# Optimization experiments

Measured on AMD Instinct MI355X. Metric: run time of the kernel, lower is better.

## Reference

```python
import jax, jax.numpy as jnp
import numpy as np

B, T, D, H = 64, 1024, 256, 256
DROP_P = 0.5


def setup_inputs() -> dict:
    key = jax.random.key(0)
    ks = jax.random.split(key, 14)
    s = 1.0 / np.sqrt(H)
    inp = {
        "x": jax.random.normal(ks[0], (B, T, D), jnp.float32),
        "W_f": jax.random.normal(ks[1], (D, 4 * H), jnp.float32) * s,
        "U_f": jax.random.normal(ks[2], (H, 4 * H), jnp.float32) * s,
        "b_f": jnp.zeros((4 * H,), jnp.float32),
        "pi_f": jax.random.normal(ks[3], (H,), jnp.float32) * s,
        "pf_f": jax.random.normal(ks[4], (H,), jnp.float32) * s,
        "po_f": jax.random.normal(ks[5], (H,), jnp.float32) * s,
        "W_b": jax.random.normal(ks[6], (D, 4 * H), jnp.float32) * s,
        "U_b": jax.random.normal(ks[7], (H, 4 * H), jnp.float32) * s,
        "b_b": jnp.zeros((4 * H,), jnp.float32),
        "pi_b": jax.random.normal(ks[8], (H,), jnp.float32) * s,
        "pf_b": jax.random.normal(ks[9], (H,), jnp.float32) * s,
        "po_b": jax.random.normal(ks[10], (H,), jnp.float32) * s,
    }
    return inp


def _peephole_lstm_dir(x, W, U, b, pi, pf, po, reverse):
    # Precompute input projection for all timesteps: [B,T,4H]
    xW = jnp.einsum('btd,dg->btg', x, W) + b
    if reverse:
        xW = xW[:, ::-1]
    h0 = jnp.zeros((x.shape[0], H), x.dtype)
    c0 = jnp.zeros((x.shape[0], H), x.dtype)

    def step(carry, xw_t):
        h, c = carry
        g = xw_t + h @ U                       # [B,4H]
        gi, gf, gg, go = jnp.split(g, 4, axis=-1)
        i = jax.nn.sigmoid(gi + pi * c)        # peephole on c_{t-1}
        f = jax.nn.sigmoid(gf + pf * c)
        c_new = f * c + i * jnp.tanh(gg)
        o = jax.nn.sigmoid(go + po * c_new)    # peephole on c_t
        h_new = o * jnp.tanh(c_new)
        return (h_new, c_new), h_new

    _, hs = jax.lax.scan(step, (h0, c0), jnp.swapaxes(xW, 0, 1))  # [T,B,H]
    hs = jnp.swapaxes(hs, 0, 1)  # [B,T,H]
    if reverse:
        hs = hs[:, ::-1]
    return hs


def reference(x, W_f, U_f, b_f, pi_f, pf_f, po_f, W_b, U_b, b_b, pi_b, pf_b, po_b):
    h_fwd = _peephole_lstm_dir(x, W_f, U_f, b_f, pi_f, pf_f, po_f, reverse=False)
    h_bwd = _peephole_lstm_dir(x, W_b, U_b, b_b, pi_b, pf_b, po_b, reverse=True)
    out = jnp.concatenate([h_fwd, h_bwd], axis=-1)  # [B,T,2H]
    # training-mode dropout with a fixed key (deterministic for baselining)
    keep = jax.random.bernoulli(jax.random.key(42), 1.0 - DROP_P, out.shape)
    out = jnp.where(keep, out / (1.0 - DROP_P), 0.0)
    return out
```

## Files before the change

### kernel.cpp

```cpp
#include <hip/hip_runtime.h>

typedef unsigned int uint;
typedef unsigned short ushort;
typedef unsigned long long u64;
typedef short bf16x8 __attribute__((ext_vector_type(8)));
typedef float f32x4 __attribute__((ext_vector_type(4)));

#define XW_OFF   0ull
#define XB_OFF   (XW_OFF + 268435456ull)
#define WT_OFF   (XB_OFF + 33554432ull)
#define UT_OFF   (WT_OFF + 1048576ull)
#define WS_NEED  (UT_OFF + 1048576ull)

static __device__ __forceinline__ ushort f2bf(float f) {
  uint u = __float_as_uint(f);
  return (ushort)((u + 0x7fffu + ((u >> 16) & 1u)) >> 16);
}
static __device__ __forceinline__ float bf2f(ushort s) {
  return __uint_as_float((uint)s << 16);
}
static __device__ __forceinline__ float fsig(float x) {
  return 1.0f / (1.0f + __expf(-x));
}
static __device__ __forceinline__ float ftanh(float x) {
  return 1.0f - 2.0f / (__expf(2.0f * x) + 1.0f);
}

static __device__ __forceinline__ void gload_lds16(const void* g, void* l) {
  auto gp = (const __attribute__((address_space(1))) uint*)((const void*)g);
  auto lp = (__attribute__((address_space(3))) uint*)((void*)l);
  __builtin_amdgcn_global_load_lds(gp, lp, 16, 0, 0);
}

__global__ __launch_bounds__(256) void k_convert(
    const float* __restrict__ x,
    const float* __restrict__ Wf, const float* __restrict__ Wb,
    const float* __restrict__ Uf, const float* __restrict__ Ub,
    ushort* __restrict__ xb, ushort* __restrict__ wt, ushort* __restrict__ ut)
{
  uint tid = blockIdx.x * 256u + threadIdx.x;
  if (tid < 2097152u) {
    uint base = tid * 8u;
    float4 a = *(const float4*)(x + base);
    float4 b = *(const float4*)(x + base + 4);
    uint4 o;
    o.x = (uint)f2bf(a.x) | ((uint)f2bf(a.y) << 16);
    o.y = (uint)f2bf(a.z) | ((uint)f2bf(a.w) << 16);
    o.z = (uint)f2bf(b.x) | ((uint)f2bf(b.y) << 16);
    o.w = (uint)f2bf(b.z) | ((uint)f2bf(b.w) << 16);
    *(uint4*)(xb + base) = o;
  } else {
    uint e = tid - 2097152u;
    uint which = e >> 18;
    uint i = e & 262143u;
    uint n = i >> 8, k = i & 255u;
    uint orig = (n & 3u) * 256u + (n >> 2);
    const float* src = (which == 0) ? Wf : (which == 1) ? Wb : (which == 2) ? Uf : Ub;
    ushort v = f2bf(src[k * 1024u + orig]);
    ushort* dst = (which < 2) ? (wt + which * 262144u) : (ut + (which - 2u) * 262144u);
    dst[n * 256u + k] = v;
  }
}

__global__ __launch_bounds__(256) void k_gemm(
    const ushort* __restrict__ xb, const ushort* __restrict__ wt,
    const float* __restrict__ biasF, const float* __restrict__ biasB,
    ushort* __restrict__ xw2)
{
  const int dir = blockIdx.z;
  const ushort* W = wt + dir * 262144;
  const float* bias = dir ? biasB : biasF;
  const int m0 = blockIdx.x * 128;
  const int n0 = blockIdx.y * 128;
  const int tid = threadIdx.x;
  const int lane = tid & 63, wave = tid >> 6;
  const int l15 = lane & 15, l4 = lane >> 4;
  const int wr = wave >> 1, wc = wave & 1;

  __shared__ __align__(16) ushort lds[17664];
  ushort* As = lds;
  ushort* Bs = lds + 5120;

  f32x4 acc[4][4] = {};
  const int arow = tid >> 1, aseg = tid & 1;

  for (int kit = 0; kit < 8; ++kit) {
    int k0 = kit * 32;
    const ushort* sa = xb + (m0 + arow) * 256 + k0 + aseg * 16;
    uint4 a0 = *(const uint4*)sa;
    uint4 a1 = *(const uint4*)(sa + 8);
    const ushort* sb = W + (n0 + arow) * 256 + k0 + aseg * 16;
    uint4 b0 = *(const uint4*)sb;
    uint4 b1 = *(const uint4*)(sb + 8);
    *(uint4*)(As + arow * 40 + aseg * 16) = a0;
    *(uint4*)(As + arow * 40 + aseg * 16 + 8) = a1;
    *(uint4*)(Bs + arow * 40 + aseg * 16) = b0;
    *(uint4*)(Bs + arow * 40 + aseg * 16 + 8) = b1;
    __syncthreads();
    bf16x8 af[4], bfr[4];
#pragma unroll
    for (int m = 0; m < 4; ++m) af[m] = *(const bf16x8*)(As + (wr * 64 + m * 16 + l15) * 40 + l4 * 8);
#pragma unroll
    for (int n = 0; n < 4; ++n) bfr[n] = *(const bf16x8*)(Bs + (wc * 64 + n * 16 + l15) * 40 + l4 * 8);
#pragma unroll
    for (int m = 0; m < 4; ++m)
#pragma unroll
      for (int n = 0; n < 4; ++n)
        acc[m][n] = __builtin_amdgcn_mfma_f32_16x16x32_bf16(af[m], bfr[n], acc[m][n], 0, 0, 0);
    __syncthreads();
  }

  float bv[4];
#pragma unroll
  for (int n = 0; n < 4; ++n) {
    int colp = n0 + wc * 64 + n * 16 + l15;
    bv[n] = bias[(colp & 3) * 256 + (colp >> 2)];
  }
  ushort* tl = lds;
#pragma unroll
  for (int m = 0; m < 4; ++m)
#pragma unroll
    for (int n = 0; n < 4; ++n) {
      int col = wc * 64 + n * 16 + l15;
#pragma unroll
      for (int r = 0; r < 4; ++r) {
        int trow = wr * 64 + m * 16 + l4 * 4 + r;
        tl[trow * 136 + col] = f2bf(acc[m][n][r] + bv[n]);
      }
    }
  __syncthreads();

  const int b = m0 >> 10;
  const int bgrp = b >> 2, b_loc = b & 3;
  const int t0 = m0 & 1023;
#pragma unroll
  for (int it = 0; it < 8; ++it) {
    int idx = it * 256 + tid;
    int row = idx >> 4, ch = idx & 15;
    uint4 v = *(const uint4*)(tl + row * 136 + ch * 8);
    u64 off = ((u64)((dir * 16 + bgrp) * 1024 + (t0 + row))) * 4096ull
              + (u64)(b_loc * 1024 + n0 + ch * 8);
    *(uint4*)(xw2 + off) = v;
  }
}

__global__ __launch_bounds__(1024) void k_rec(
    const ushort* __restrict__ xw2, const ushort* __restrict__ ut,
    const float* __restrict__ pif, const float* __restrict__ pff, const float* __restrict__ pof,
    const float* __restrict__ pib, const float* __restrict__ pfb, const float* __restrict__ pob,
    float* __restrict__ out)
{
  const int bid = blockIdx.x;
  const int dir = bid >> 4;
  const int bgrp = bid & 15;
  const int tid = threadIdx.x;
  const int lane = tid & 63, wv = tid >> 6;
  const int l15 = lane & 15, l4 = lane >> 4;
  const int u = wv * 16 + l15;

  __shared__ __align__(16) ushort uld[65536];
  __shared__ __align__(16) ushort hst[2176];
  __shared__ __align__(16) ushort xsl[12288];

  const float* piP = dir ? pib : pif;
  const float* pfP = dir ? pfb : pff;
  const float* poP = dir ? pob : pof;
  const float ppi = piP[u], ppf = pfP[u], ppo = poP[u];

  const ushort* U = ut + dir * 262144;
  bf16x8 ufr[6][4];
#pragma unroll
  for (int g = 0; g < 4; ++g) {
    const ushort* up = U + (u * 4 + g) * 256;
#pragma unroll
    for (int kt = 0; kt < 6; ++kt)
      ufr[kt][g] = *(const bf16x8*)(up + kt * 32 + l4 * 8);
#pragma unroll
    for (int kt = 6; kt < 8; ++kt)
      *(bf16x8*)(uld + wv * 4096 + ((kt - 6) * 4 + g) * 512 + lane * 8) =
          *(const bf16x8*)(up + kt * 32 + l4 * 8);
  }
  for (int i = tid; i < 2176; i += 1024) hst[i] = 0;

  const ushort* xwbase = xw2 + (u64)(dir * 16 + bgrp) * 1024ull * 4096ull;

  if (tid < 512) {
    const ushort* s0 = xwbase + (u64)(dir ? 1023 : 0) * 4096ull + (uint)tid * 8u;
    const ushort* s1 = xwbase + (u64)(dir ? 1022 : 1) * 4096ull + (uint)tid * 8u;
    gload_lds16(s0, &xsl[(tid >> 6) * 512]);
    gload_lds16(s1, &xsl[4096 + (tid >> 6) * 512]);
  }
  asm volatile("s_waitcnt vmcnt(0) lgkmcnt(0)" ::: "memory");
  __syncthreads();

  float cr = 0.f;
  float* outp = out + ((u64)(bgrp * 4 + l4) * 1024ull) * 512ull + (u64)(dir * 256 + u);
  int scur = 0;

  for (int t = 0; t < 1024; ++t) {
    if (t + 2 < 1024 && tid < 512) {
      const int snxt = (scur >= 1) ? (scur - 1) : 2;
      const ushort* src = xwbase + (u64)(dir ? 1021 - t : t + 2) * 4096ull + (uint)tid * 8u;
      gload_lds16(src, &xsl[snxt * 4096 + (tid >> 6) * 512]);
    }

    const ushort* sA = hst + ((t + 1) & 1) * 1088 + (l15 >> 2) * 272 + l4 * 8;
    f32x4 acc0 = {0.f, 0.f, 0.f, 0.f}, acc1 = acc0, acc2 = acc0, acc3 = acc0;
#pragma unroll
    for (int kt = 0; kt < 6; ++kt) {
      bf16x8 a = *(const bf16x8*)(sA + kt * 32);
      acc0 = __builtin_amdgcn_mfma_f32_16x16x32_bf16(a, ufr[kt][0], acc0, 0, 0, 0);
      acc1 = __builtin_amdgcn_mfma_f32_16x16x32_bf16(a, ufr[kt][1], acc1, 0, 0, 0);
      acc2 = __builtin_amdgcn_mfma_f32_16x16x32_bf16(a, ufr[kt][2], acc2, 0, 0, 0);
      acc3 = __builtin_amdgcn_mfma_f32_16x16x32_bf16(a, ufr[kt][3], acc3, 0, 0, 0);
    }
#pragma unroll
    for (int kt = 6; kt < 8; ++kt) {
      bf16x8 a = *(const bf16x8*)(sA + kt * 32);
      const ushort* ub = uld + wv * 4096 + (kt - 6) * 2048 + lane * 8;
      acc0 = __builtin_amdgcn_mfma_f32_16x16x32_bf16(a, *(const bf16x8*)(ub), acc0, 0, 0, 0);
      acc1 = __builtin_amdgcn_mfma_f32_16x16x32_bf16(a, *(const bf16x8*)(ub + 512), acc1, 0, 0, 0);
      acc2 = __builtin_amdgcn_mfma_f32_16x16x32_bf16(a, *(const bf16x8*)(ub + 1024), acc2, 0, 0, 0);
      acc3 = __builtin_amdgcn_mfma_f32_16x16x32_bf16(a, *(const bf16x8*)(ub + 1536), acc3, 0, 0, 0);
    }

    u64 xv = *(const u64*)(xsl + scur * 4096 + (l4 << 10) + (u << 2));
    {
      float cc = cr;
      float gi = acc0[0] + bf2f((ushort)xv);
      float gf = acc1[0] + bf2f((ushort)(xv >> 16));
      float gg = acc2[0] + bf2f((ushort)(xv >> 32));
      float go = acc3[0] + bf2f((ushort)(xv >> 48));
      float iv = fsig(gi + ppi * cc);
      float fv = fsig(gf + ppf * cc);
      float cn = fv * cc + iv * ftanh(gg);
      float ov = fsig(go + ppo * cn);
      float h = ov * ftanh(cn);
      cr = cn;
      hst[(t & 1) * 1088 + l4 * 272 + u] = f2bf(h);
      const int tout = dir ? (1023 - t) : t;
      __builtin_nontemporal_store(h, outp + (u64)tout * 512ull);
    }

    asm volatile("s_waitcnt vmcnt(2) lgkmcnt(0)\n\ts_barrier" ::: "memory");
    scur = (scur == 2) ? 0 : (scur + 1);
  }
}

#define TFR(r) { x0 += x1; x1 = (x1 << (r)) | (x1 >> (32 - (r))); x1 ^= x0; }
#define RND4A TFR(13) TFR(15) TFR(26) TFR(6)
#define RND4B TFR(17) TFR(29) TFR(16) TFR(24)

static __device__ __forceinline__ void threefry(uint c0, uint c1, uint& y0, uint& y1) {
  const uint k0 = 0u, k1 = 42u;
  const uint ks2 = k0 ^ k1 ^ 0x1BD11BDAu;
  uint x0 = c0 + k0, x1 = c1 + k1;
  RND4A x0 += k1;  x1 += ks2 + 1u;
  RND4B x0 += ks2; x1 += k0 + 2u;
  RND4A x0 += k0;  x1 += k1 + 3u;
  RND4B x0 += k1;  x1 += ks2 + 4u;
  RND4A x0 += ks2; x1 += k0 + 5u;
  y0 = x0; y1 = x1;
}

__global__ __launch_bounds__(256) void k_drop(float* out, uint n) {
  uint i = blockIdx.x * 256u + threadIdx.x;
  if (i < n) {
    uint y0, y1;
    threefry(0u, i, y0, y1);
    uint w = y0 ^ y1;
    float v = out[i];
    out[i] = (w >> 31) ? 0.0f : v * 2.0f;
  }
}

extern "C" void kernel_launch(void* const* d_in, const int* in_sizes, int n_in,
                              void* d_out, int out_size, void* d_ws, size_t ws_size,
                              hipStream_t stream)
{
  const float* x   = (const float*)d_in[0];
  const float* Wf  = (const float*)d_in[1];
  const float* Uf  = (const float*)d_in[2];
  const float* bf_ = (const float*)d_in[3];
  const float* pif = (const float*)d_in[4];
  const float* pff = (const float*)d_in[5];
  const float* pof = (const float*)d_in[6];
  const float* Wb  = (const float*)d_in[7];
  const float* Ub  = (const float*)d_in[8];
  const float* bb_ = (const float*)d_in[9];
  const float* pib = (const float*)d_in[10];
  const float* pfb = (const float*)d_in[11];
  const float* pob = (const float*)d_in[12];
  float* out = (float*)d_out;
  char* ws = (char*)d_ws;

  if (ws_size < WS_NEED) {
    hipMemsetAsync(d_out, 0, (size_t)out_size * 4, stream);
    return;
  }

  ushort* xwp = (ushort*)(ws + XW_OFF);
  ushort* xbp = (ushort*)(ws + XB_OFF);
  ushort* wtp = (ushort*)(ws + WT_OFF);
  ushort* utp = (ushort*)(ws + UT_OFF);

  k_convert<<<12288, 256, 0, stream>>>(x, Wf, Wb, Uf, Ub, xbp, wtp, utp);
  k_gemm<<<dim3(512, 8, 2), 256, 0, stream>>>(xbp, wtp, bf_, bb_, xwp);
  k_rec<<<32, 1024, 0, stream>>>(xwp, utp, pif, pff, pof, pib, pfb, pob, out);
  k_drop<<<(out_size + 255) / 256, 256, 0, stream>>>(out, (uint)out_size);
}
```

Before: 2.647 ms.

## Keep all recurrent weights in registers and prefetch xW directly into registers

The full U slice (all 8 k-tiles across 4 gates) is now held in VGPRs instead of splitting 2 k-tiles into LDS. The async global-to-LDS triple buffer for the precomputed input projection is replaced by a two-deep per-thread register prefetch. The timestep loop is unrolled by two, and output stores become ordinary stores instead of nontemporal ones. The aim is to drop LDS reads of U and xW from the serial critical path. With 1024-thread blocks, the extra 32 VGPRs of weights per thread risks spilling to scratch, which would sit inside the recurrence loop.

```diff
diff --git a/kernel.cpp b/kernel.cpp
--- a/kernel.cpp
+++ b/kernel.cpp
@@ -24,12 +24,6 @@
 }
 static __device__ __forceinline__ float ftanh(float x) {
   return 1.0f - 2.0f / (__expf(2.0f * x) + 1.0f);
-}
-
-static __device__ __forceinline__ void gload_lds16(const void* g, void* l) {
-  auto gp = (const __attribute__((address_space(1))) uint*)((const void*)g);
-  auto lp = (__attribute__((address_space(3))) uint*)((void*)l);
-  __builtin_amdgcn_global_load_lds(gp, lp, 16, 0, 0);
 }
 
 __global__ __launch_bounds__(256) void k_convert(
@@ -154,13 +148,11 @@
   const int dir = bid >> 4;
   const int bgrp = bid & 15;
   const int tid = threadIdx.x;
-  const int lane = tid & 63, wv = tid >> 6;
+  const int lane = tid & 63;
   const int l15 = lane & 15, l4 = lane >> 4;
-  const int u = wv * 16 + l15;
-
-  __shared__ __align__(16) ushort uld[65536];
+  const int u = (tid >> 6) * 16 + l15;
+
   __shared__ __align__(16) ushort hst[2176];
-  __shared__ __align__(16) ushort xsl[12288];
 
   const float* piP = dir ? pib : pif;
   const float* pfP = dir ? pfb : pff;
@@ -168,82 +160,67 @@
   const float ppi = piP[u], ppf = pfP[u], ppo = poP[u];
 
   const ushort* U = ut + dir * 262144;
-  bf16x8 ufr[6][4];
+  bf16x8 ufr[8][4];
 #pragma unroll
   for (int g = 0; g < 4; ++g) {
     const ushort* up = U + (u * 4 + g) * 256;
 #pragma unroll
-    for (int kt = 0; kt < 6; ++kt)
+    for (int kt = 0; kt < 8; ++kt)
       ufr[kt][g] = *(const bf16x8*)(up + kt * 32 + l4 * 8);
-#pragma unroll
-    for (int kt = 6; kt < 8; ++kt)
-      *(bf16x8*)(uld + wv * 4096 + ((kt - 6) * 4 + g) * 512 + lane * 8) =
-          *(const bf16x8*)(up + kt * 32 + l4 * 8);
   }
   for (int i = tid; i < 2176; i += 1024) hst[i] = 0;
-
-  const ushort* xwbase = xw2 + (u64)(dir * 16 + bgrp) * 1024ull * 4096ull;
-
-  if (tid < 512) {
-    const ushort* s0 = xwbase + (u64)(dir ? 1023 : 0) * 4096ull + (uint)tid * 8u;
-    const ushort* s1 = xwbase + (u64)(dir ? 1022 : 1) * 4096ull + (uint)tid * 8u;
-    gload_lds16(s0, &xsl[(tid >> 6) * 512]);
-    gload_lds16(s1, &xsl[4096 + (tid >> 6) * 512]);
-  }
-  asm volatile("s_waitcnt vmcnt(0) lgkmcnt(0)" ::: "memory");
   __syncthreads();
 
+  const ushort* xp = xw2 + (u64)(dir * 16 + bgrp) * 4194304ull
+                     + (uint)(l4 * 1024 + u * 4);
   float cr = 0.f;
   float* outp = out + ((u64)(bgrp * 4 + l4) * 1024ull) * 512ull + (u64)(dir * 256 + u);
-  int scur = 0;
-
-  for (int t = 0; t < 1024; ++t) {
-    if (t + 2 < 1024 && tid < 512) {
-      const int snxt = (scur >= 1) ? (scur - 1) : 2;
-      const ushort* src = xwbase + (u64)(dir ? 1021 - t : t + 2) * 4096ull + (uint)tid * 8u;
-      gload_lds16(src, &xsl[snxt * 4096 + (tid >> 6) * 512]);
-    }
-
+
+  u64 pa = *(const u64*)(xp + (u64)(dir ? 1023 : 0) * 4096ull);
+  u64 pb = *(const u64*)(xp + (u64)(dir ? 1022 : 1) * 4096ull);
+
+  auto step = [&](u64 xv, int t) {
     const ushort* sA = hst + ((t + 1) & 1) * 1088 + (l15 >> 2) * 272 + l4 * 8;
     f32x4 acc0 = {0.f, 0.f, 0.f, 0.f}, acc1 = acc0, acc2 = acc0, acc3 = acc0;
 #pragma unroll
-    for (int kt = 0; kt < 6; ++kt) {
+    for (int kt = 0; kt < 8; ++kt) {
       bf16x8 a = *(const bf16x8*)(sA + kt * 32);
       acc0 = __builtin_amdgcn_mfma_f32_16x16x32_bf16(a, ufr[kt][0], acc0, 0, 0, 0);
       acc1 = __builtin_amdgcn_mfma_f32_16x16x32_bf16(a, ufr[kt][1], acc1, 0, 0, 0);
       acc2 = __builtin_amdgcn_mfma_f32_16x16x32_bf16(a, ufr[kt][2], acc2, 0, 0, 0);
       acc3 = __builtin_amdgcn_mfma_f32_16x16x32_bf16(a, ufr[kt][3], acc3, 0, 0, 0);
     }
-#pragma unroll
-    for (int kt = 6; kt < 8; ++kt) {
-      bf16x8 a = *(const bf16x8*)(sA + kt * 32);
-      const ushort* ub = uld + wv * 4096 + (kt - 6) * 2048 + lane * 8;
-      acc0 = __builtin_amdgcn_mfma_f32_16x16x32_bf16(a, *(const bf16x8*)(ub), acc0, 0, 0, 0);
-      acc1 = __builtin_amdgcn_mfma_f32_16x16x32_bf16(a, *(const bf16x8*)(ub + 512), acc1, 0, 0, 0);
-      acc2 = __builtin_amdgcn_mfma_f32_16x16x32_bf16(a, *(const bf16x8*)(ub + 1024), acc2, 0, 0, 0);
-      acc3 = __builtin_amdgcn_mfma_f32_16x16x32_bf16(a, *(const bf16x8*)(ub + 1536), acc3, 0, 0, 0);
-    }
-
-    u64 xv = *(const u64*)(xsl + scur * 4096 + (l4 << 10) + (u << 2));
+    float cc = cr;
+    float gi = acc0[0] + bf2f((ushort)xv);
+    float gf = acc1[0] + bf2f((ushort)(xv >> 16));
+    float gg = acc2[0] + bf2f((ushort)(xv >> 32));
+    float go = acc3[0] + bf2f((ushort)(xv >> 48));
+    float iv = fsig(gi + ppi * cc);
+    float fv = fsig(gf + ppf * cc);
+    float cn = fv * cc + iv * ftanh(gg);
+    float ov = fsig(go + ppo * cn);
+    float h = ov * ftanh(cn);
+    cr = cn;
+    hst[(t & 1) * 1088 + l4 * 272 + u] = f2bf(h);
+    const int tout = dir ? (1023 - t) : t;
+    outp[(u64)tout * 512ull] = h;
+  };
+
+  for (int t = 0; t < 1024; t += 2) {
     {
-      float cc = cr;
-      float gi = acc0[0] + bf2f((ushort)xv);
-      float gf = acc1[0] + bf2f((ushort)(xv >> 16));
-      float gg = acc2[0] + bf2f((ushort)(xv >> 32));
-      float go = acc3[0] + bf2f((ushort)(xv >> 48));
-      float iv = fsig(gi + ppi * cc);
-      float fv = fsig(gf + ppf * cc);
-      float cn = fv * cc + iv * ftanh(gg);
-      float ov = fsig(go + ppo * cn);
-      float h = ov * ftanh(cn);
-      cr = cn;
-      hst[(t & 1) * 1088 + l4 * 272 + u] = f2bf(h);
-      const int tout = dir ? (1023 - t) : t;
-      __builtin_nontemporal_store(h, outp + (u64)tout * 512ull);
-    }
-
-    asm volatile("s_waitcnt vmcnt(2) lgkmcnt(0)\n\ts_barrier" ::: "memory");
-    scur = (scur == 2) ? 0 : (scur + 1);
+      u64 xv = pa;
+      if (t + 2 < 1024)
+        pa = *(const u64*)(xp + (u64)(dir ? 1021 - t : t + 2) * 4096ull);
+      step(xv, t);
+      asm volatile("s_waitcnt vmcnt(2) lgkmcnt(0)\n\ts_barrier" ::: "memory");
+    }
+    {
+      u64 xv = pb;
+      if (t + 3 < 1024)
+        pb = *(const u64*)(xp + (u64)(dir ? 1020 - t : t + 3) * 4096ull);
+      step(xv, t + 1);
+      asm volatile("s_waitcnt vmcnt(2) lgkmcnt(0)\n\ts_barrier" ::: "memory");
+    }
   }
 }
 
```

New measurement: 5.825 ms. 120% more time.

## Halve recurrent block to 512 threads, keep full U slice in registers

Applied to the files above, without the earlier changes.

The recurrent kernel now runs 8 waves per block instead of 16, and each wave handles 32 hidden units with 8 MFMA accumulators. The entire U slice (8x8 bf16x8 fragments per lane) lives in registers, which removes the LDS-resident part of U and its per-step LDS reads. The U transpose layout in the convert kernel is changed to match the new wave-to-unit mapping, and the xW prefetch is moved after the gate math with a waitcnt adjusted to match. The cost is much higher register pressure (launch_bounds 512,2) and half as many waves to hide latency in the serial loop, with the output store changed from nontemporal to a plain store.

```diff
diff --git a/kernel.cpp b/kernel.cpp
--- a/kernel.cpp
+++ b/kernel.cpp
@@ -54,7 +54,13 @@
     uint which = e >> 18;
     uint i = e & 262143u;
     uint n = i >> 8, k = i & 255u;
-    uint orig = (n & 3u) * 256u + (n >> 2);
+    uint orig;
+    if (which < 2) {
+      orig = (n & 3u) * 256u + (n >> 2);
+    } else {
+      uint w = n >> 7, nn = (n >> 4) & 7u, c = n & 15u;
+      orig = (nn & 3u) * 256u + w * 32u + ((nn >> 2) << 4) + c;
+    }
     const float* src = (which == 0) ? Wf : (which == 1) ? Wb : (which == 2) ? Uf : Ub;
     ushort v = f2bf(src[k * 1024u + orig]);
     ushort* dst = (which < 2) ? (wt + which * 262144u) : (ut + (which - 2u) * 262144u);
@@ -144,7 +150,7 @@
   }
 }
 
-__global__ __launch_bounds__(1024) void k_rec(
+__global__ __launch_bounds__(512, 2) void k_rec(
     const ushort* __restrict__ xw2, const ushort* __restrict__ ut,
     const float* __restrict__ pif, const float* __restrict__ pff, const float* __restrict__ pof,
     const float* __restrict__ pib, const float* __restrict__ pfb, const float* __restrict__ pob,
@@ -156,35 +162,32 @@
   const int tid = threadIdx.x;
   const int lane = tid & 63, wv = tid >> 6;
   const int l15 = lane & 15, l4 = lane >> 4;
-  const int u = wv * 16 + l15;
-
-  __shared__ __align__(16) ushort uld[65536];
+  const int u0 = wv * 32 + l15;
+  const int u1 = u0 + 16;
+
   __shared__ __align__(16) ushort hst[2176];
   __shared__ __align__(16) ushort xsl[12288];
 
   const float* piP = dir ? pib : pif;
   const float* pfP = dir ? pfb : pff;
   const float* poP = dir ? pob : pof;
-  const float ppi = piP[u], ppf = pfP[u], ppo = poP[u];
+  const float pi0 = piP[u0], pf0 = pfP[u0], po0 = poP[u0];
+  const float pi1 = piP[u1], pf1 = pfP[u1], po1 = poP[u1];
 
   const ushort* U = ut + dir * 262144;
-  bf16x8 ufr[6][4];
-#pragma unroll
-  for (int g = 0; g < 4; ++g) {
-    const ushort* up = U + (u * 4 + g) * 256;
-#pragma unroll
-    for (int kt = 0; kt < 6; ++kt)
-      ufr[kt][g] = *(const bf16x8*)(up + kt * 32 + l4 * 8);
-#pragma unroll
-    for (int kt = 6; kt < 8; ++kt)
-      *(bf16x8*)(uld + wv * 4096 + ((kt - 6) * 4 + g) * 512 + lane * 8) =
-          *(const bf16x8*)(up + kt * 32 + l4 * 8);
-  }
-  for (int i = tid; i < 2176; i += 1024) hst[i] = 0;
-
-  const ushort* xwbase = xw2 + (u64)(dir * 16 + bgrp) * 1024ull * 4096ull;
-
-  if (tid < 512) {
+  bf16x8 ufr[8][8];
+#pragma unroll
+  for (int n = 0; n < 8; ++n) {
+    const ushort* up = U + (wv * 128 + n * 16 + l15) * 256;
+#pragma unroll
+    for (int kt = 0; kt < 8; ++kt)
+      ufr[kt][n] = *(const bf16x8*)(up + kt * 32 + l4 * 8);
+  }
+  for (int i = tid; i < 2176; i += 512) hst[i] = 0;
+
+  const ushort* xwbase = xw2 + (u64)(dir * 16 + bgrp) * 4194304ull;
+
+  {
     const ushort* s0 = xwbase + (u64)(dir ? 1023 : 0) * 4096ull + (uint)tid * 8u;
     const ushort* s1 = xwbase + (u64)(dir ? 1022 : 1) * 4096ull + (uint)tid * 8u;
     gload_lds16(s0, &xsl[(tid >> 6) * 512]);
@@ -193,57 +196,70 @@
   asm volatile("s_waitcnt vmcnt(0) lgkmcnt(0)" ::: "memory");
   __syncthreads();
 
-  float cr = 0.f;
-  float* outp = out + ((u64)(bgrp * 4 + l4) * 1024ull) * 512ull + (u64)(dir * 256 + u);
-  int scur = 0;
+  float cr0 = 0.f, cr1 = 0.f;
+  float* outb = out + (u64)(bgrp * 4 + l4) * 524288ull + (u64)(dir * 256);
+  int s_r = 0, s_w = 2;
 
   for (int t = 0; t < 1024; ++t) {
-    if (t + 2 < 1024 && tid < 512) {
-      const int snxt = (scur >= 1) ? (scur - 1) : 2;
-      const ushort* src = xwbase + (u64)(dir ? 1021 - t : t + 2) * 4096ull + (uint)tid * 8u;
-      gload_lds16(src, &xsl[snxt * 4096 + (tid >> 6) * 512]);
-    }
-
     const ushort* sA = hst + ((t + 1) & 1) * 1088 + (l15 >> 2) * 272 + l4 * 8;
     f32x4 acc0 = {0.f, 0.f, 0.f, 0.f}, acc1 = acc0, acc2 = acc0, acc3 = acc0;
-#pragma unroll
-    for (int kt = 0; kt < 6; ++kt) {
+    f32x4 acc4 = acc0, acc5 = acc0, acc6 = acc0, acc7 = acc0;
+#pragma unroll
+    for (int kt = 0; kt < 8; ++kt) {
       bf16x8 a = *(const bf16x8*)(sA + kt * 32);
       acc0 = __builtin_amdgcn_mfma_f32_16x16x32_bf16(a, ufr[kt][0], acc0, 0, 0, 0);
       acc1 = __builtin_amdgcn_mfma_f32_16x16x32_bf16(a, ufr[kt][1], acc1, 0, 0, 0);
       acc2 = __builtin_amdgcn_mfma_f32_16x16x32_bf16(a, ufr[kt][2], acc2, 0, 0, 0);
       acc3 = __builtin_amdgcn_mfma_f32_16x16x32_bf16(a, ufr[kt][3], acc3, 0, 0, 0);
-    }
-#pragma unroll
-    for (int kt = 6; kt < 8; ++kt) {
-      bf16x8 a = *(const bf16x8*)(sA + kt * 32);
-      const ushort* ub = uld + wv * 4096 + (kt - 6) * 2048 + lane * 8;
-      acc0 = __builtin_amdgcn_mfma_f32_16x16x32_bf16(a, *(const bf16x8*)(ub), acc0, 0, 0, 0);
-      acc1 = __builtin_amdgcn_mfma_f32_16x16x32_bf16(a, *(const bf16x8*)(ub + 512), acc1, 0, 0, 0);
-      acc2 = __builtin_amdgcn_mfma_f32_16x16x32_bf16(a, *(const bf16x8*)(ub + 1024), acc2, 0, 0, 0);
-      acc3 = __builtin_amdgcn_mfma_f32_16x16x32_bf16(a, *(const bf16x8*)(ub + 1536), acc3, 0, 0, 0);
-    }
-
-    u64 xv = *(const u64*)(xsl + scur * 4096 + (l4 << 10) + (u << 2));
+      acc4 = __builtin_amdgcn_mfma_f32_16x16x32_bf16(a, ufr[kt][4], acc4, 0, 0, 0);
+      acc5 = __builtin_amdgcn_mfma_f32_16x16x32_bf16(a, ufr[kt][5], acc5, 0, 0, 0);
+      acc6 = __builtin_amdgcn_mfma_f32_16x16x32_bf16(a, ufr[kt][6], acc6, 0, 0, 0);
+      acc7 = __builtin_amdgcn_mfma_f32_16x16x32_bf16(a, ufr[kt][7], acc7, 0, 0, 0);
+    }
+
+    const int tout = dir ? (1023 - t) : t;
+    u64 xv0 = *(const u64*)(xsl + s_r * 4096 + (l4 << 10) + (u0 << 2));
+    u64 xv1 = *(const u64*)(xsl + s_r * 4096 + (l4 << 10) + (u1 << 2));
     {
-      float cc = cr;
-      float gi = acc0[0] + bf2f((ushort)xv);
-      float gf = acc1[0] + bf2f((ushort)(xv >> 16));
-      float gg = acc2[0] + bf2f((ushort)(xv >> 32));
-      float go = acc3[0] + bf2f((ushort)(xv >> 48));
-      float iv = fsig(gi + ppi * cc);
-      float fv = fsig(gf + ppf * cc);
+      float cc = cr0;
+      float gi = acc0[0] + bf2f((ushort)xv0);
+      float gf = acc1[0] + bf2f((ushort)(xv0 >> 16));
+      float gg = acc2[0] + bf2f((ushort)(xv0 >> 32));
+      float go = acc3[0] + bf2f((ushort)(xv0 >> 48));
+      float iv = fsig(gi + pi0 * cc);
+      float fv = fsig(gf + pf0 * cc);
       float cn = fv * cc + iv * ftanh(gg);
-      float ov = fsig(go + ppo * cn);
+      float ov = fsig(go + po0 * cn);
       float h = ov * ftanh(cn);
-      cr = cn;
-      hst[(t & 1) * 1088 + l4 * 272 + u] = f2bf(h);
-      const int tout = dir ? (1023 - t) : t;
-      __builtin_nontemporal_store(h, outp + (u64)tout * 512ull);
-    }
-
-    asm volatile("s_waitcnt vmcnt(2) lgkmcnt(0)\n\ts_barrier" ::: "memory");
-    scur = (scur == 2) ? 0 : (scur + 1);
+      cr0 = cn;
+      hst[(t & 1) * 1088 + l4 * 272 + u0] = f2bf(h);
+      outb[(u64)tout * 512ull + (u64)u0] = h;
+    }
+    {
+      float cc = cr1;
+      float gi = acc4[0] + bf2f((ushort)xv1);
+      float gf = acc5[0] + bf2f((ushort)(xv1 >> 16));
+      float gg = acc6[0] + bf2f((ushort)(xv1 >> 32));
+      float go = acc7[0] + bf2f((ushort)(xv1 >> 48));
+      float iv = fsig(gi + pi1 * cc);
+      float fv = fsig(gf + pf1 * cc);
+      float cn = fv * cc + iv * ftanh(gg);
+      float ov = fsig(go + po1 * cn);
+      float h = ov * ftanh(cn);
+      cr1 = cn;
+      hst[(t & 1) * 1088 + l4 * 272 + u1] = f2bf(h);
+      outb[(u64)tout * 512ull + (u64)u1] = h;
+    }
+
+    {
+      const int tn = (t + 2 < 1024) ? t + 2 : 1023;
+      const ushort* src = xwbase + (u64)(dir ? 1023 - tn : tn) * 4096ull + (uint)tid * 8u;
+      gload_lds16(src, &xsl[s_w * 4096 + (tid >> 6) * 512]);
+    }
+
+    asm volatile("s_waitcnt vmcnt(3) lgkmcnt(0)\n\ts_barrier" ::: "memory");
+    s_r = (s_r == 2) ? 0 : s_r + 1;
+    s_w = (s_w == 2) ? 0 : s_w + 1;
   }
 }
 
@@ -306,6 +322,6 @@
 
   k_convert<<<12288, 256, 0, stream>>>(x, Wf, Wb, Uf, Ub, xbp, wtp, utp);
   k_gemm<<<dim3(512, 8, 2), 256, 0, stream>>>(xbp, wtp, bf_, bb_, xwp);
-  k_rec<<<32, 1024, 0, stream>>>(xwp, utp, pif, pff, pof, pib, pfb, pob, out);
+  k_rec<<<32, 512, 0, stream>>>(xwp, utp, pif, pff, pof, pib, pfb, pob, out);
   k_drop<<<(out_size + 255) / 256, 256, 0, stream>>>(out, (uint)out_size);
 }
```

New measurement: 4.497 ms. 1.7x slower.

## Keep all recurrent weights in registers and make async loads uniform across waves

Applied to the files above, without the earlier changes.

Moves the last two K-tiles of the recurrent weight matrix from LDS into registers, so every wave holds all 8x4 bf16 fragments and the per-step LDS reads of U go away. The prefetch is made uniform: every thread issues an LDS-direct load each step (upper threads write into a scratch buffer), which keeps the vmcnt(2) wait consistent across waves. Nontemporal output stores become plain stores. The cost is much higher register pressure (128 VGPRs of weights per thread at 1024 threads per block), which risks spills, plus extra dummy global loads every step.

```diff
diff --git a/kernel.cpp b/kernel.cpp
--- a/kernel.cpp
+++ b/kernel.cpp
@@ -158,9 +158,9 @@
   const int l15 = lane & 15, l4 = lane >> 4;
   const int u = wv * 16 + l15;
 
-  __shared__ __align__(16) ushort uld[65536];
   __shared__ __align__(16) ushort hst[2176];
   __shared__ __align__(16) ushort xsl[12288];
+  __shared__ __align__(16) ushort trash[512];
 
   const float* piP = dir ? pib : pif;
   const float* pfP = dir ? pfb : pff;
@@ -168,21 +168,17 @@
   const float ppi = piP[u], ppf = pfP[u], ppo = poP[u];
 
   const ushort* U = ut + dir * 262144;
-  bf16x8 ufr[6][4];
+  bf16x8 ufr[8][4];
 #pragma unroll
   for (int g = 0; g < 4; ++g) {
     const ushort* up = U + (u * 4 + g) * 256;
 #pragma unroll
-    for (int kt = 0; kt < 6; ++kt)
+    for (int kt = 0; kt < 8; ++kt)
       ufr[kt][g] = *(const bf16x8*)(up + kt * 32 + l4 * 8);
-#pragma unroll
-    for (int kt = 6; kt < 8; ++kt)
-      *(bf16x8*)(uld + wv * 4096 + ((kt - 6) * 4 + g) * 512 + lane * 8) =
-          *(const bf16x8*)(up + kt * 32 + l4 * 8);
   }
   for (int i = tid; i < 2176; i += 1024) hst[i] = 0;
 
-  const ushort* xwbase = xw2 + (u64)(dir * 16 + bgrp) * 1024ull * 4096ull;
+  const ushort* xwbase = xw2 + (u64)(dir * 16 + bgrp) * 4194304ull;
 
   if (tid < 512) {
     const ushort* s0 = xwbase + (u64)(dir ? 1023 : 0) * 4096ull + (uint)tid * 8u;
@@ -195,36 +191,29 @@
 
   float cr = 0.f;
   float* outp = out + ((u64)(bgrp * 4 + l4) * 1024ull) * 512ull + (u64)(dir * 256 + u);
-  int scur = 0;
+  int s_r = 0, s_w = 2;
 
   for (int t = 0; t < 1024; ++t) {
-    if (t + 2 < 1024 && tid < 512) {
-      const int snxt = (scur >= 1) ? (scur - 1) : 2;
-      const ushort* src = xwbase + (u64)(dir ? 1021 - t : t + 2) * 4096ull + (uint)tid * 8u;
-      gload_lds16(src, &xsl[snxt * 4096 + (tid >> 6) * 512]);
+    if (tid < 512) {
+      const int tn = (t + 2 < 1024) ? t + 2 : 1023;
+      const ushort* src = xwbase + (u64)(dir ? 1023 - tn : tn) * 4096ull + (uint)tid * 8u;
+      gload_lds16(src, &xsl[s_w * 4096 + (tid >> 6) * 512]);
+    } else {
+      gload_lds16(xwbase + (uint)lane * 8u, trash);
     }
 
     const ushort* sA = hst + ((t + 1) & 1) * 1088 + (l15 >> 2) * 272 + l4 * 8;
     f32x4 acc0 = {0.f, 0.f, 0.f, 0.f}, acc1 = acc0, acc2 = acc0, acc3 = acc0;
 #pragma unroll
-    for (int kt = 0; kt < 6; ++kt) {
+    for (int kt = 0; kt < 8; ++kt) {
       bf16x8 a = *(const bf16x8*)(sA + kt * 32);
       acc0 = __builtin_amdgcn_mfma_f32_16x16x32_bf16(a, ufr[kt][0], acc0, 0, 0, 0);
       acc1 = __builtin_amdgcn_mfma_f32_16x16x32_bf16(a, ufr[kt][1], acc1, 0, 0, 0);
       acc2 = __builtin_amdgcn_mfma_f32_16x16x32_bf16(a, ufr[kt][2], acc2, 0, 0, 0);
       acc3 = __builtin_amdgcn_mfma_f32_16x16x32_bf16(a, ufr[kt][3], acc3, 0, 0, 0);
     }
-#pragma unroll
-    for (int kt = 6; kt < 8; ++kt) {
-      bf16x8 a = *(const bf16x8*)(sA + kt * 32);
-      const ushort* ub = uld + wv * 4096 + (kt - 6) * 2048 + lane * 8;
-      acc0 = __builtin_amdgcn_mfma_f32_16x16x32_bf16(a, *(const bf16x8*)(ub), acc0, 0, 0, 0);
-      acc1 = __builtin_amdgcn_mfma_f32_16x16x32_bf16(a, *(const bf16x8*)(ub + 512), acc1, 0, 0, 0);
-      acc2 = __builtin_amdgcn_mfma_f32_16x16x32_bf16(a, *(const bf16x8*)(ub + 1024), acc2, 0, 0, 0);
-      acc3 = __builtin_amdgcn_mfma_f32_16x16x32_bf16(a, *(const bf16x8*)(ub + 1536), acc3, 0, 0, 0);
-    }
-
-    u64 xv = *(const u64*)(xsl + scur * 4096 + (l4 << 10) + (u << 2));
+
+    u64 xv = *(const u64*)(xsl + s_r * 4096 + (l4 << 10) + (u << 2));
     {
       float cc = cr;
       float gi = acc0[0] + bf2f((ushort)xv);
@@ -239,11 +228,12 @@
       cr = cn;
       hst[(t & 1) * 1088 + l4 * 272 + u] = f2bf(h);
       const int tout = dir ? (1023 - t) : t;
-      __builtin_nontemporal_store(h, outp + (u64)tout * 512ull);
+      outp[(u64)tout * 512ull] = h;
     }
 
     asm volatile("s_waitcnt vmcnt(2) lgkmcnt(0)\n\ts_barrier" ::: "memory");
-    scur = (scur == 2) ? 0 : (scur + 1);
+    s_r = (s_r == 2) ? 0 : s_r + 1;
+    s_w = (s_w == 2) ? 0 : s_w + 1;
   }
 }
 
```

Result: slower. 5.488 ms (+107.4%).
